# Performance work log

Measured on AMD Instinct MI355X. Metric: run time of the kernel, lower is better.

Reference implementation:

```python
import jax, jax.numpy as jnp
import numpy as np

CAUSAL = True

def setup_inputs() -> dict:
    key = jax.random.key(0)
    kq, kk, kv = jax.random.split(key, 3)
    B, S, H, D = 2, 2048, 16, 64
    q = jax.random.normal(kq, (B, S, H, D), dtype=jnp.float32)
    k = jax.random.normal(kk, (B, S, H, D), dtype=jnp.float32)
    v = jax.random.normal(kv, (B, S, H, D), dtype=jnp.float32)
    return {"q": q, "k": k, "v": v}

def reference(q, k, v):
    # q,k,v: [B, S, H, D]
    B, Sq, H, D = q.shape
    Sk = k.shape[1]
    scale = 1.0 / jnp.sqrt(jnp.asarray(D, dtype=q.dtype))
    # scores: [B, H, Sq, Sk]
    scores = jnp.einsum('bqhd,bkhd->bhqk', q * scale, k)
    if CAUSAL:
        causal_mask = jnp.triu(jnp.ones((Sq, Sk), dtype=bool), k=1)
        scores = jnp.where(causal_mask, -jnp.inf, scores)
    attn = jax.nn.softmax(scores, axis=-1)
    # output: [B, Sq, H, D]
    out = jnp.einsum('bhqk,bkhd->bqhd', attn, v)
    return out
```

## Files before the change

kernel.cpp:

```cpp
#include <hip/hip_runtime.h>


typedef __bf16  bf16x8_t  __attribute__((ext_vector_type(8)));
typedef short   short4_t  __attribute__((ext_vector_type(4)));
typedef float   f32x4     __attribute__((ext_vector_type(4)));

#define MFMA_K32(a, b, c) __builtin_amdgcn_mfma_f32_16x16x32_bf16((a), (b), (c), 0, 0, 0)

__device__ __forceinline__ f32x4 mfma_k16(short4_t a, short4_t b, f32x4 c) {
#if defined(__HIP_DEVICE_COMPILE__)
    return __builtin_amdgcn_mfma_f32_16x16x16bf16_1k(a, b, c, 0, 0, 0);
#else
    return c;
#endif
}

constexpr int   SEQ = 2048, NH = 16;
constexpr int   SROW = NH * 64;
constexpr float QS   = 0.125f * 1.44269504088896f;

__device__ __forceinline__ unsigned f2bfu(float f) {
    unsigned u = __builtin_bit_cast(unsigned, f);
    return (u + 0x7fffu + ((u >> 16) & 1u)) >> 16;
}
__device__ __forceinline__ unsigned pk2(float x, float y) {
#if defined(__HIP_DEVICE_COMPILE__) && __has_builtin(__builtin_amdgcn_cvt_pk_bf16_f32)
    typedef __bf16 bfv2 __attribute__((ext_vector_type(2)));
    bfv2 v = __builtin_amdgcn_cvt_pk_bf16_f32(x, y);
    return __builtin_bit_cast(unsigned, v);
#else
    return (f2bfu(x) & 0xffffu) | (f2bfu(y) << 16);
#endif
}

__global__ __launch_bounds__(256) void prepack(const float* __restrict__ K,
                                               const float* __restrict__ V,
                                               unsigned short* __restrict__ Kp,
                                               unsigned short* __restrict__ Vp) {
    const int blk = blockIdx.x;
    const int tid = threadIdx.x;
    if (blk < 1024) {
        const int bh = blk >> 5, c = blk & 31;
        const int b  = bh >> 4,  h = bh & 15;
        const int nt = tid >> 6, lane = tid & 63;
        const int llo = lane & 15, lhi = lane >> 4;
        const float* src = K + (size_t)(b * SEQ + c * 64 + nt * 16 + llo) * SROW + h * 64;
#pragma unroll
        for (int ks = 0; ks < 2; ++ks) {
            const float4* p = (const float4*)(src + ks * 32 + lhi * 8);
            float4 a = p[0], d4 = p[1];
            uint4 u;
            u.x = pk2(a.x, a.y);   u.y = pk2(a.z, a.w);
            u.z = pk2(d4.x, d4.y); u.w = pk2(d4.z, d4.w);
            *(uint4*)(Kp + (size_t)(bh * 32 + c) * 4096 + (nt * 2 + ks) * 512 + lane * 8) = u;
        }
    } else {
        const int q  = blk - 1024;
        const int bh = q >> 5, c = q & 31;
        const int b  = bh >> 4, h = bh & 15;
        const int dt = tid >> 6, lane = tid & 63;
        const int llo = lane & 15, lhi = lane >> 4;
        const float* src = V + (size_t)(b * SEQ + c * 64 + lhi * 4) * SROW + h * 64 + dt * 16 + llo;
#pragma unroll
        for (int kq = 0; kq < 4; ++kq) {
            const float* s2 = src + (size_t)(kq * 16) * SROW;
            float f0 = s2[0], f1 = s2[SROW], f2 = s2[2 * SROW], f3 = s2[3 * SROW];
            uint2 u;
            u.x = pk2(f0, f1); u.y = pk2(f2, f3);
            *(uint2*)(Vp + (size_t)(bh * 32 + c) * 4096 + (kq * 4 + dt) * 256 + lane * 4) = u;
        }
    }
}

__global__ __launch_bounds__(256, 4) void fa_fwd(const float* __restrict__ Q,
                                                 const unsigned short* __restrict__ Kp,
                                                 const unsigned short* __restrict__ Vp,
                                                 float* __restrict__ O) {
    const int id = blockIdx.x;
    const int bh = id & 31;
    const int pr = id >> 5;
    const int b  = bh >> 4, h = bh & 15;
    const int T0 = 63 - pr;
    const int T1 = pr;
    const int split = (T0 >> 1) + 1;

    const int tid  = threadIdx.x;
    const int w    = tid >> 6;
    const int lane = tid & 63;
    const int lhi  = lane >> 4;
    const int llo  = lane & 15;

    __shared__ __align__(16) float Red[4][5][64][4];

    const unsigned short* Kbh = Kp + (size_t)bh * (32 * 4096);
    const unsigned short* Vbh = Vp + (size_t)bh * (32 * 4096);

    const int koff0 = (w * 2 + 0) * 512 + lane * 8;
    const int koff1 = (w * 2 + 1) * 512 + lane * 8;
    const int voff  = (w * 4) * 256 + lane * 4;

    bf16x8_t qf[2][2];
    auto loadQ = [&](int Tq) {
#pragma unroll
        for (int mt = 0; mt < 2; ++mt)
#pragma unroll
            for (int ks = 0; ks < 2; ++ks) {
                const float* qp = Q + (size_t)(b * SEQ + Tq * 32 + mt * 16 + llo) * SROW + h * 64 + ks * 32 + lhi * 8;
                float4 a = ((const float4*)qp)[0], c4 = ((const float4*)qp)[1];
                uint4 u;
                u.x = pk2(a.x * QS, a.y * QS); u.y = pk2(a.z * QS, a.w * QS);
                u.z = pk2(c4.x * QS, c4.y * QS); u.w = pk2(c4.z * QS, c4.w * QS);
                qf[mt][ks] = __builtin_bit_cast(bf16x8_t, u);
            }
    };

    f32x4 acc[2][4], accL[2];
    auto clearAcc = [&]() {
#pragma unroll
        for (int mt = 0; mt < 2; ++mt) {
            accL[mt] = (f32x4){0.f, 0.f, 0.f, 0.f};
#pragma unroll
            for (int dt = 0; dt < 4; ++dt) acc[mt][dt] = (f32x4){0.f, 0.f, 0.f, 0.f};
        }
    };

    auto finish = [&](int Tq) {
        const int q0 = Tq * 32;
#pragma unroll
        for (int mt = 0; mt < 2; ++mt) {
#pragma unroll
            for (int dt = 0; dt < 4; ++dt) *(f32x4*)&Red[w][dt][lane][0] = acc[mt][dt];
            *(f32x4*)&Red[w][4][lane][0] = accL[mt];
            __syncthreads();
            f32x4 oc = (f32x4){0.f, 0.f, 0.f, 0.f};
            f32x4 ls = (f32x4){0.f, 0.f, 0.f, 0.f};
#pragma unroll
            for (int u = 0; u < 4; ++u) {
                oc += *(const f32x4*)&Red[u][w][lane][0];
                ls += *(const f32x4*)&Red[u][4][lane][0];
            }
#pragma unroll
            for (int r = 0; r < 4; ++r)
                O[(size_t)(b * SEQ + q0 + mt * 16 + lhi * 4 + r) * SROW + h * 64 + w * 16 + llo] = oc[r] / ls[r];
            __syncthreads();
        }
    };

    loadQ(T0);
    clearAcc();

    short4_t ones;
#pragma unroll
    for (int j = 0; j < 4; ++j) ones[j] = (short)0x3F80;

    uint4 kc0 = *(const uint4*)(Kbh + koff0);
    uint4 kc1 = *(const uint4*)(Kbh + koff1);

    for (int it = 0; it < 33; ++it) {
        const int ph = (it >= split);

        if (it == split) {
            finish(T0);
            clearAcc();
            loadQ(T1);
        }

        const int kt  = ph ? it - split : it;
        const int q0  = (ph ? T1 : T0) * 32;
        const int kv0 = kt * 64;
        const size_t cb = (size_t)kt * 4096;

        uint4 kn0, kn1;
        const bool more = (it + 1 < 33);
        if (more) {
            const int ktn = (it + 1 >= split) ? (it + 1 - split) : (it + 1);
            kn0 = *(const uint4*)(Kbh + (size_t)ktn * 4096 + koff0);
            kn1 = *(const uint4*)(Kbh + (size_t)ktn * 4096 + koff1);
        }
        uint2 vc[4];
#pragma unroll
        for (int dt = 0; dt < 4; ++dt)
            vc[dt] = *(const uint2*)(Vbh + cb + voff + dt * 256);

        f32x4 s[2];
#pragma unroll
        for (int mt = 0; mt < 2; ++mt) {
            f32x4 z = (f32x4){0.f, 0.f, 0.f, 0.f};
            z = MFMA_K32(__builtin_bit_cast(bf16x8_t, kc0), qf[mt][0], z);
            z = MFMA_K32(__builtin_bit_cast(bf16x8_t, kc1), qf[mt][1], z);
            s[mt] = z;
        }

#pragma unroll
        for (int mt = 0; mt < 2; ++mt) {
            if (kv0 + w * 16 + 15 > q0 + mt * 16) {
                const int m_g = q0 + mt * 16 + llo;
#pragma unroll
                for (int r = 0; r < 4; ++r)
                    if (kv0 + w * 16 + lhi * 4 + r > m_g) s[mt][r] = -INFINITY;
            }
        }

        short4_t pf[2];
#pragma unroll
        for (int mt = 0; mt < 2; ++mt) {
            uint2 u = make_uint2(
                pk2(__builtin_amdgcn_exp2f(s[mt][0]), __builtin_amdgcn_exp2f(s[mt][1])),
                pk2(__builtin_amdgcn_exp2f(s[mt][2]), __builtin_amdgcn_exp2f(s[mt][3])));
            pf[mt] = __builtin_bit_cast(short4_t, u);
        }

#pragma unroll
        for (int dt = 0; dt < 4; ++dt) {
            short4_t vf = __builtin_bit_cast(short4_t, vc[dt]);
            acc[0][dt] = mfma_k16(pf[0], vf, acc[0][dt]);
            acc[1][dt] = mfma_k16(pf[1], vf, acc[1][dt]);
        }
        accL[0] = mfma_k16(pf[0], ones, accL[0]);
        accL[1] = mfma_k16(pf[1], ones, accL[1]);

        if (more) { kc0 = kn0; kc1 = kn1; }
    }

    finish(T1);
}

extern "C" void kernel_launch(void* const* d_in, const int* in_sizes, int n_in,
                              void* d_out, int out_size, void* d_ws, size_t ws_size,
                              hipStream_t stream) {
    const float* q = (const float*)d_in[0];
    const float* k = (const float*)d_in[1];
    const float* v = (const float*)d_in[2];
    float* o = (float*)d_out;
    unsigned short* Kp = (unsigned short*)d_ws;
    unsigned short* Vp = Kp + (size_t)32 * 32 * 4096;
    prepack<<<dim3(2048), dim3(256), 0, stream>>>(k, v, Kp, Vp);
    fa_fwd<<<dim3(1024), dim3(256), 0, stream>>>(q, Kp, Vp, o);
}
```

Measured before the change: 125.8 us.

## Replace paired causal tiles per block with one tile per block, double grid

Each block previously handled two complementary query tiles (T and 63-T) to balance causal work across 33 iterations. Now each block handles a single 32-row query tile with a variable iteration count. The grid doubles to 2048 blocks, heaviest tiles are dispatched first, and launch bounds ask for 8 blocks per CU. This removes the mid-loop finish and reload and gives more parallelism. The cost is relying on the hardware scheduler for load balance, plus possible register pressure from the higher occupancy target.

```diff
diff --git a/kernel.cpp b/kernel.cpp
--- a/kernel.cpp
+++ b/kernel.cpp
@@ -72,17 +72,16 @@
     }
 }
 
-__global__ __launch_bounds__(256, 4) void fa_fwd(const float* __restrict__ Q,
+__global__ __launch_bounds__(256, 8) void fa_fwd(const float* __restrict__ Q,
                                                  const unsigned short* __restrict__ Kp,
                                                  const unsigned short* __restrict__ Vp,
                                                  float* __restrict__ O) {
     const int id = blockIdx.x;
     const int bh = id & 31;
-    const int pr = id >> 5;
+    const int T  = 63 - (id >> 5);
     const int b  = bh >> 4, h = bh & 15;
-    const int T0 = 63 - pr;
-    const int T1 = pr;
-    const int split = (T0 >> 1) + 1;
+    const int iters = (T >> 1) + 1;
+    const int q0    = T * 32;
 
     const int tid  = threadIdx.x;
     const int w    = tid >> 6;
@@ -100,54 +99,25 @@
     const int voff  = (w * 4) * 256 + lane * 4;
 
     bf16x8_t qf[2][2];
-    auto loadQ = [&](int Tq) {
-#pragma unroll
-        for (int mt = 0; mt < 2; ++mt)
-#pragma unroll
-            for (int ks = 0; ks < 2; ++ks) {
-                const float* qp = Q + (size_t)(b * SEQ + Tq * 32 + mt * 16 + llo) * SROW + h * 64 + ks * 32 + lhi * 8;
-                float4 a = ((const float4*)qp)[0], c4 = ((const float4*)qp)[1];
-                uint4 u;
-                u.x = pk2(a.x * QS, a.y * QS); u.y = pk2(a.z * QS, a.w * QS);
-                u.z = pk2(c4.x * QS, c4.y * QS); u.w = pk2(c4.z * QS, c4.w * QS);
-                qf[mt][ks] = __builtin_bit_cast(bf16x8_t, u);
-            }
-    };
+#pragma unroll
+    for (int mt = 0; mt < 2; ++mt)
+#pragma unroll
+        for (int ks = 0; ks < 2; ++ks) {
+            const float* qp = Q + (size_t)(b * SEQ + q0 + mt * 16 + llo) * SROW + h * 64 + ks * 32 + lhi * 8;
+            float4 a = ((const float4*)qp)[0], c4 = ((const float4*)qp)[1];
+            uint4 u;
+            u.x = pk2(a.x * QS, a.y * QS); u.y = pk2(a.z * QS, a.w * QS);
+            u.z = pk2(c4.x * QS, c4.y * QS); u.w = pk2(c4.z * QS, c4.w * QS);
+            qf[mt][ks] = __builtin_bit_cast(bf16x8_t, u);
+        }
 
     f32x4 acc[2][4], accL[2];
-    auto clearAcc = [&]() {
-#pragma unroll
-        for (int mt = 0; mt < 2; ++mt) {
-            accL[mt] = (f32x4){0.f, 0.f, 0.f, 0.f};
-#pragma unroll
-            for (int dt = 0; dt < 4; ++dt) acc[mt][dt] = (f32x4){0.f, 0.f, 0.f, 0.f};
-        }
-    };
-
-    auto finish = [&](int Tq) {
-        const int q0 = Tq * 32;
-#pragma unroll
-        for (int mt = 0; mt < 2; ++mt) {
-#pragma unroll
-            for (int dt = 0; dt < 4; ++dt) *(f32x4*)&Red[w][dt][lane][0] = acc[mt][dt];
-            *(f32x4*)&Red[w][4][lane][0] = accL[mt];
-            __syncthreads();
-            f32x4 oc = (f32x4){0.f, 0.f, 0.f, 0.f};
-            f32x4 ls = (f32x4){0.f, 0.f, 0.f, 0.f};
-#pragma unroll
-            for (int u = 0; u < 4; ++u) {
-                oc += *(const f32x4*)&Red[u][w][lane][0];
-                ls += *(const f32x4*)&Red[u][4][lane][0];
-            }
-#pragma unroll
-            for (int r = 0; r < 4; ++r)
-                O[(size_t)(b * SEQ + q0 + mt * 16 + lhi * 4 + r) * SROW + h * 64 + w * 16 + llo] = oc[r] / ls[r];
-            __syncthreads();
-        }
-    };
-
-    loadQ(T0);
-    clearAcc();
+#pragma unroll
+    for (int mt = 0; mt < 2; ++mt) {
+        accL[mt] = (f32x4){0.f, 0.f, 0.f, 0.f};
+#pragma unroll
+        for (int dt = 0; dt < 4; ++dt) acc[mt][dt] = (f32x4){0.f, 0.f, 0.f, 0.f};
+    }
 
     short4_t ones;
 #pragma unroll
@@ -156,26 +126,15 @@
     uint4 kc0 = *(const uint4*)(Kbh + koff0);
     uint4 kc1 = *(const uint4*)(Kbh + koff1);
 
-    for (int it = 0; it < 33; ++it) {
-        const int ph = (it >= split);
-
-        if (it == split) {
-            finish(T0);
-            clearAcc();
-            loadQ(T1);
-        }
-
-        const int kt  = ph ? it - split : it;
-        const int q0  = (ph ? T1 : T0) * 32;
+    for (int kt = 0; kt < iters; ++kt) {
         const int kv0 = kt * 64;
         const size_t cb = (size_t)kt * 4096;
 
         uint4 kn0, kn1;
-        const bool more = (it + 1 < 33);
+        const bool more = (kt + 1 < iters);
         if (more) {
-            const int ktn = (it + 1 >= split) ? (it + 1 - split) : (it + 1);
-            kn0 = *(const uint4*)(Kbh + (size_t)ktn * 4096 + koff0);
-            kn1 = *(const uint4*)(Kbh + (size_t)ktn * 4096 + koff1);
+            kn0 = *(const uint4*)(Kbh + cb + 4096 + koff0);
+            kn1 = *(const uint4*)(Kbh + cb + 4096 + koff1);
         }
         uint2 vc[4];
 #pragma unroll
@@ -222,7 +181,24 @@
         if (more) { kc0 = kn0; kc1 = kn1; }
     }
 
-    finish(T1);
+#pragma unroll
+    for (int mt = 0; mt < 2; ++mt) {
+#pragma unroll
+        for (int dt = 0; dt < 4; ++dt) *(f32x4*)&Red[w][dt][lane][0] = acc[mt][dt];
+        *(f32x4*)&Red[w][4][lane][0] = accL[mt];
+        __syncthreads();
+        f32x4 oc = (f32x4){0.f, 0.f, 0.f, 0.f};
+        f32x4 ls = (f32x4){0.f, 0.f, 0.f, 0.f};
+#pragma unroll
+        for (int u = 0; u < 4; ++u) {
+            oc += *(const f32x4*)&Red[u][w][lane][0];
+            ls += *(const f32x4*)&Red[u][4][lane][0];
+        }
+#pragma unroll
+        for (int r = 0; r < 4; ++r)
+            O[(size_t)(b * SEQ + q0 + mt * 16 + lhi * 4 + r) * SROW + h * 64 + w * 16 + llo] = oc[r] / ls[r];
+        __syncthreads();
+    }
 }
 
 extern "C" void kernel_launch(void* const* d_in, const int* in_sizes, int n_in,
@@ -235,5 +211,5 @@
     unsigned short* Kp = (unsigned short*)d_ws;
     unsigned short* Vp = Kp + (size_t)32 * 32 * 4096;
     prepack<<<dim3(2048), dim3(256), 0, stream>>>(k, v, Kp, Vp);
-    fa_fwd<<<dim3(1024), dim3(256), 0, stream>>>(q, Kp, Vp, o);
-}
+    fa_fwd<<<dim3(2048), dim3(256), 0, stream>>>(q, Kp, Vp, o);
+}
```

After: 350.6 us. +178.7%, slower.
